# Optimization experiments

Hardware: AMD Instinct MI355X
Metric: run time of the kernel (lower is better)

## Reference

```python
import jax, jax.numpy as jnp
import numpy as np

H = 16          # num_attention_heads
D = 1024        # input_size == hidden_size
HD = D // H     # attention_head_size = 64
EPS = 1e-12


def setup_inputs() -> dict:
    key = jax.random.key(0)
    ks = jax.random.split(key, 12)
    B, S = 4, 2048
    sc = 1.0 / np.sqrt(D)
    return {
        "x": jax.random.normal(ks[0], (B, S, D), jnp.float32),
        "y": jax.random.normal(ks[1], (B, S, D), jnp.float32),
        "Wq": jax.random.normal(ks[2], (D, D), jnp.float32) * sc,
        "bq": jnp.zeros((D,), jnp.float32),
        "Wk": jax.random.normal(ks[3], (D, D), jnp.float32) * sc,
        "bk": jnp.zeros((D,), jnp.float32),
        "Wv": jax.random.normal(ks[4], (D, D), jnp.float32) * sc,
        "bv": jnp.zeros((D,), jnp.float32),
        "Wd": jax.random.normal(ks[5], (D, D), jnp.float32) * sc,
        "bd": jnp.zeros((D,), jnp.float32),
        "gamma": jnp.ones((D,), jnp.float32),
        "beta": jnp.zeros((D,), jnp.float32),
        "debug": 0,
    }


def _split_heads(t):
    B, S, _ = t.shape
    return t.reshape(B, S, H, HD).transpose(0, 2, 1, 3)  # [B,H,S,hd]


def reference(x, y, Wq, bq, Wk, bk, Wv, bv, Wd, bd, gamma, beta, debug):
    # torch Linear: t @ W.T + b
    q = _split_heads(x @ Wq.T + bq)   # query from x
    k = _split_heads(y @ Wk.T + bk)   # key from y
    v = _split_heads(x @ Wv.T + bv)   # value from x (as in source)
    scores = jnp.einsum("bhqd,bhkd->bhqk", q, k) / np.sqrt(HD)
    probs = jax.nn.softmax(scores, axis=-1)  # dropout: eval mode (identity)
    ctx = jnp.einsum("bhqk,bhkd->bhqd", probs, v)
    B, _, S, _ = ctx.shape
    ctx = ctx.transpose(0, 2, 1, 3).reshape(B, S, D)
    h = ctx @ Wd.T + bd               # out_dropout: eval mode (identity)
    h = h + x
    u = h.mean(-1, keepdims=True)
    s = jnp.square(h - u).mean(-1, keepdims=True)
    h = (h - u) / jnp.sqrt(s + EPS)
    return gamma * h + beta
```

## Files before the change

### kernel.cpp

```cpp
#include <hip/hip_runtime.h>
#include <hip/hip_bf16.h>
#include <stdint.h>


typedef unsigned short ushortT;
typedef __attribute__((ext_vector_type(8))) __bf16 bf16x8;
typedef __attribute__((ext_vector_type(4))) float f32x4;
typedef __attribute__((ext_vector_type(16))) float f32x16;
typedef __attribute__((ext_vector_type(8))) unsigned short ushort8;
typedef __attribute__((ext_vector_type(4))) unsigned short ushort4v;

__device__ __forceinline__ unsigned short f2bf(float f) {
  union { float f; unsigned u; } x; x.f = f;
  unsigned r = (x.u + 0x7FFFu + ((x.u >> 16) & 1u)) >> 16;
  return (unsigned short)r;
}

__device__ __forceinline__ unsigned cvtpk_bf16(float lo, float hi) {
  unsigned r;
  asm("v_cvt_pk_bf16_f32 %0, %1, %2" : "=v"(r) : "v"(lo), "v"(hi));
  return r;
}

__device__ __forceinline__ void load_lds16(const void* g, void* l) {
  __builtin_amdgcn_global_load_lds(
      (const __attribute__((address_space(1))) void*)g,
      (__attribute__((address_space(3))) void*)l, 16, 0, 0);
}

__device__ __forceinline__ f32x4 mfma16(bf16x8 a, bf16x8 b, f32x4 c) {
  return __builtin_amdgcn_mfma_f32_16x16x32_bf16(a, b, c, 0, 0, 0);
}
__device__ __forceinline__ f32x16 mfma32(bf16x8 a, bf16x8 b, f32x16 c) {
  return __builtin_amdgcn_mfma_f32_32x32x16_bf16(a, b, c, 0, 0, 0);
}

__global__ __launch_bounds__(256) void k_cvt_all(
    const float* __restrict__ x, const float* __restrict__ y,
    const float* __restrict__ w0, const float* __restrict__ w1,
    const float* __restrict__ w2, const float* __restrict__ w3,
    ushortT* __restrict__ ox, ushortT* __restrict__ oy,
    ushortT* __restrict__ o0, ushortT* __restrict__ o1,
    ushortT* __restrict__ o2, ushortT* __restrict__ o3) {
  int b = blockIdx.x;
  const float* in;
  ushortT* out;
  int blk;
  if (b < 4096) {
    in = x; out = ox; blk = b;
  } else if (b < 8192) {
    in = y; out = oy; blk = b - 4096;
  } else {
    int z = (b - 8192) >> 9;
    blk = (b - 8192) & 511;
    in = (z == 0) ? w0 : (z == 1) ? w1 : (z == 2) ? w2 : w3;
    out = (z == 0) ? o0 : (z == 1) ? o1 : (z == 2) ? o2 : o3;
  }
  int i = blk * 256 + threadIdx.x;
  const float4* p = (const float4*)in;
  float4 u = p[(size_t)i * 2];
  float4 v = p[(size_t)i * 2 + 1];
  ushort8 o;
  o[0] = f2bf(u.x); o[1] = f2bf(u.y); o[2] = f2bf(u.z); o[3] = f2bf(u.w);
  o[4] = f2bf(v.x); o[5] = f2bf(v.y); o[6] = f2bf(v.z); o[7] = f2bf(v.w);
  *(ushort8*)(out + (size_t)i * 8) = o;
}

__global__ __launch_bounds__(512, 4) void k_gemm(
    const ushortT* __restrict__ xbf, const ushortT* __restrict__ ybf,
    const ushortT* __restrict__ wq, const ushortT* __restrict__ wk,
    const ushortT* __restrict__ wv, const ushortT* __restrict__ wd,
    const float* __restrict__ bq, const float* __restrict__ bk,
    const float* __restrict__ bv, const float* __restrict__ bd,
    const ushortT* __restrict__ ctx, const float* __restrict__ xres,
    ushortT* __restrict__ Qo, ushortT* __restrict__ Ko,
    ushortT* __restrict__ Vt, float* __restrict__ Ho, int mode_base) {
  __shared__ ushortT lA[2][128 * 64];
  __shared__ ushortT lB[2][128 * 64];
  const int t = threadIdx.x;
  const int lane = t & 63;
  const int w = t >> 6;
  const int wm = w >> 1, wn = w & 1;
  const int mode = mode_base + blockIdx.z;
  const int flat = blockIdx.x + (blockIdx.y << 3);
  const int xcd = flat & 7, j = flat >> 3;
  const int m0 = (xcd * 8 + (j >> 3)) * 128;
  const int n0 = (j & 7) * 128;

  const ushortT* A = (mode == 1) ? ybf : (mode == 3 ? ctx : xbf);
  const ushortT* W = (mode == 0) ? wq : (mode == 1 ? wk : (mode == 2 ? wv : wd));
  const float* bias = (mode == 0) ? bq : (mode == 1 ? bk : (mode == 2 ? bv : bd));

  f32x4 z = {0.f, 0.f, 0.f, 0.f};
  f32x4 acc[2][4];
#pragma unroll
  for (int i = 0; i < 2; ++i)
#pragma unroll
    for (int j2 = 0; j2 < 4; ++j2) acc[i][j2] = z;

  const int so = t * 16;
  const int srow = so >> 7;
  const int skb = (so & 127) ^ ((srow & 7) << 4);
  const ushortT* asrc = A + (size_t)(m0 + srow) * 1024 + (skb >> 1);
  const ushortT* wsrc = W + (size_t)(n0 + srow) * 1024 + (skb >> 1);

#define GSTAGE(buf, k0)                                                     \
  do {                                                                      \
    _Pragma("unroll")                                                       \
    for (int c = 0; c < 2; ++c) {                                           \
      load_lds16(asrc + (k0) + (size_t)c * 64 * 1024,                       \
                 (char*)&lA[buf][0] + c * 8192 + t * 16);                   \
      load_lds16(wsrc + (k0) + (size_t)c * 64 * 1024,                       \
                 (char*)&lB[buf][0] + c * 8192 + t * 16);                   \
    }                                                                       \
  } while (0)

  GSTAGE(0, 0);
  __syncthreads();
  int cur = 0;
  for (int k0 = 0; k0 < 1024; k0 += 64) {
    if (k0 + 64 < 1024) GSTAGE(cur ^ 1, k0 + 64);
#pragma unroll
    for (int kk = 0; kk < 2; ++kk) {
      bf16x8 af[2], bfr[4];
#pragma unroll
      for (int i = 0; i < 2; ++i) {
        int arow = wm * 32 + i * 16 + (lane & 15);
        int ak = ((kk * 32 + (lane >> 4) * 8) * 2) ^ ((arow & 7) << 4);
        af[i] = *(const bf16x8*)((const char*)&lA[cur][0] + arow * 128 + ak);
      }
#pragma unroll
      for (int i = 0; i < 4; ++i) {
        int brow = wn * 64 + i * 16 + (lane & 15);
        int bk2 = ((kk * 32 + (lane >> 4) * 8) * 2) ^ ((brow & 7) << 4);
        bfr[i] = *(const bf16x8*)((const char*)&lB[cur][0] + brow * 128 + bk2);
      }
      __builtin_amdgcn_s_setprio(1);
#pragma unroll
      for (int i = 0; i < 2; ++i)
#pragma unroll
        for (int j2 = 0; j2 < 4; ++j2)
          acc[i][j2] = mfma16(af[i], bfr[j2], acc[i][j2]);
      __builtin_amdgcn_s_setprio(0);
    }
    __syncthreads();
    cur ^= 1;
  }
#undef GSTAGE

  const int cm = wm * 32 + (lane >> 4) * 4;
  const int cn = wn * 64 + (lane & 15);
  if (mode == 3) {
#pragma unroll
    for (int mi = 0; mi < 2; ++mi)
#pragma unroll
      for (int ni = 0; ni < 4; ++ni) {
        int n = n0 + cn + ni * 16;
        float bn = bias[n];
#pragma unroll
        for (int r = 0; r < 4; ++r) {
          int m = m0 + cm + mi * 16 + r;
          Ho[(size_t)m * 1024 + n] =
              acc[mi][ni][r] + bn + xres[(size_t)m * 1024 + n];
        }
      }
  } else if (mode == 2) {
#pragma unroll
    for (int mi = 0; mi < 2; ++mi)
#pragma unroll
      for (int ni = 0; ni < 4; ++ni) {
        int n = n0 + cn + ni * 16;
        int hh = n >> 6, hd = n & 63;
        float bn = bias[n];
        int m_ = m0 + cm + mi * 16;
        int b = m_ >> 11, s = m_ & 2047;
        ushort4v pk;
#pragma unroll
        for (int r = 0; r < 4; ++r) pk[r] = f2bf(acc[mi][ni][r] + bn);
        *(ushort4v*)&Vt[(((size_t)(b * 16 + hh) * 64 + hd) << 11) + s] = pk;
      }
  } else {
    ushortT* O = (mode == 0) ? Qo : Ko;
    const float qs = (mode == 0) ? 0.18033688011112042f : 1.0f;
#pragma unroll
    for (int mi = 0; mi < 2; ++mi)
#pragma unroll
      for (int ni = 0; ni < 4; ++ni) {
        int n = n0 + cn + ni * 16;
        int hh = n >> 6, hd = n & 63;
        float bn = bias[n];
#pragma unroll
        for (int r = 0; r < 4; ++r) {
          int m = m0 + cm + mi * 16 + r;
          int b = m >> 11, s = m & 2047;
          O[(((size_t)(b * 16 + hh) * 2048 + s) << 6) + hd] =
              f2bf((acc[mi][ni][r] + bn) * qs);
        }
      }
  }
}

__global__ __launch_bounds__(256, 4) void k_attn(const ushortT* __restrict__ Q,
                                                 const ushortT* __restrict__ K,
                                                 const ushortT* __restrict__ Vt,
                                                 ushortT* __restrict__ ctx) {
  __shared__ ushortT lK[2][4096];
  __shared__ ushortT lV[2][4096];
  const int t = threadIdx.x, lane = t & 63, w = t >> 6;
  const int hi = lane >> 5, l31 = lane & 31;
  const int i0 = blockIdx.x;
  const int xcd = i0 & 7, j0 = i0 >> 3;
  const int bh = xcd * 8 + (j0 >> 4);
  const int qt = j0 & 15;
  const int q0 = qt * 128 + w * 32;

  const ushortT* Qb = Q + ((size_t)bh * 2048 + q0) * 64;
  const ushortT* Kb = K + (size_t)bh * 2048 * 64;
  const ushortT* Vb = Vt + (size_t)bh * 64 * 2048;

  bf16x8 qf[4];
#pragma unroll
  for (int dc = 0; dc < 4; ++dc)
    qf[dc] = *(const bf16x8*)(Qb + l31 * 64 + dc * 16 + hi * 8);

  union { unsigned short us[8]; bf16x8 v; } ones_u;
#pragma unroll
  for (int i = 0; i < 8; ++i) ones_u.us[i] = 0x3F80;

  f32x16 accO0, accO1, accL;
#pragma unroll
  for (int i = 0; i < 16; ++i) { accO0[i] = 0.f; accO1[i] = 0.f; accL[i] = 0.f; }

  const int srow = t >> 3;
  const int scolb = ((t & 7) * 16) ^ ((srow & 7) << 4);
  const ushortT* ksrc = Kb + srow * 64 + (scolb >> 1);
  const ushortT* vsrc = Vb + (size_t)srow * 2048 + (scolb >> 1);
  const int swz = (lane & 7) << 4;
  const int hs = (hi * 16) ^ swz;
  const int krowb = l31 * 128;

#define STAGE(buf, kk)                                                        \
  do {                                                                        \
    load_lds16(ksrc + (size_t)(kk) * 64, (char*)&lK[buf][0] + w * 1024);      \
    load_lds16(ksrc + 2048 + (size_t)(kk) * 64,                               \
               (char*)&lK[buf][0] + 4096 + w * 1024);                         \
    load_lds16(vsrc + (kk), (char*)&lV[buf][0] + w * 1024);                   \
    load_lds16(vsrc + 65536 + (kk), (char*)&lV[buf][0] + 4096 + w * 1024);    \
  } while (0)

  STAGE(0, 0);
  __syncthreads();
  int cur = 0;
  for (int k0 = 0; k0 < 2048; k0 += 64) {
    if (k0 + 64 < 2048) STAGE(cur ^ 1, k0 + 64);
    const char* lKc = (const char*)&lK[cur][0];
    const char* lVc = (const char*)&lV[cur][0];
#pragma unroll
    for (int kb = 0; kb < 2; ++kb) {
      f32x16 sc;
#pragma unroll
      for (int i = 0; i < 16; ++i) sc[i] = 0.f;
      __builtin_amdgcn_s_setprio(1);
#pragma unroll
      for (int dc = 0; dc < 4; ++dc) {
        bf16x8 kf = *(const bf16x8*)(lKc + kb * 4096 + krowb + ((dc * 32) ^ hs));
        sc = mfma32(kf, qf[dc], sc);
      }
      __builtin_amdgcn_s_setprio(0);
      float p[16];
#pragma unroll
      for (int r = 0; r < 16; ++r) p[r] = __builtin_amdgcn_exp2f(sc[r]);
      union { unsigned u[4]; bf16x8 v; } pa0, pa1;
#pragma unroll
      for (int i = 0; i < 4; ++i) {
        int base = (i >> 1) * 8 + (i & 1) * 2;
        unsigned a = cvtpk_bf16(p[base], p[base + 1]);
        unsigned b = cvtpk_bf16(p[base + 4], p[base + 5]);
        asm("v_permlane32_swap_b32 %0, %1" : "+v"(a), "+v"(b));
        if (i >> 1) { pa1.u[i & 1] = a; pa1.u[2 + (i & 1)] = b; }
        else        { pa0.u[i & 1] = a; pa0.u[2 + (i & 1)] = b; }
      }
      __builtin_amdgcn_s_setprio(1);
#pragma unroll
      for (int nb = 0; nb < 2; ++nb) {
        const char* vrow = lVc + (nb * 32 + l31) * 128;
        bf16x8 vf0 = *(const bf16x8*)(vrow + ((kb * 64) ^ hs));
        bf16x8 vf1 = *(const bf16x8*)(vrow + ((kb * 64 + 32) ^ hs));
        f32x16& ao = nb ? accO1 : accO0;
        ao = mfma32(pa0.v, vf0, ao);
        ao = mfma32(pa1.v, vf1, ao);
      }
      accL = mfma32(pa0.v, ones_u.v, accL);
      accL = mfma32(pa1.v, ones_u.v, accL);
      __builtin_amdgcn_s_setprio(0);
    }
    __syncthreads();
    cur ^= 1;
  }
#undef STAGE

  int b = bh >> 4, hh = bh & 15;
  ushortT* cb = ctx + ((size_t)(b * 2048 + q0)) * 1024 + hh * 64;
#pragma unroll
  for (int r = 0; r < 16; ++r) {
    int qm = (r & 3) + 8 * (r >> 2) + 4 * hi;
    float lr = 1.0f / accL[r];
    size_t rb = (size_t)qm * 1024;
    cb[rb + l31] = f2bf(accO0[r] * lr);
    cb[rb + 32 + l31] = f2bf(accO1[r] * lr);
  }
}

__global__ __launch_bounds__(256) void k_ln(const float* __restrict__ Hi,
                                            const float* __restrict__ gamma,
                                            const float* __restrict__ beta,
                                            float* __restrict__ out) {
  const int row = blockIdx.x, t = threadIdx.x, lane = t & 63, w = t >> 6;
  const float4* hp = (const float4*)(Hi + (size_t)row * 1024);
  float4 v = hp[t];
  float s1 = v.x + v.y + v.z + v.w;
  float s2 = v.x * v.x + v.y * v.y + v.z * v.z + v.w * v.w;
#pragma unroll
  for (int off = 1; off < 64; off <<= 1) {
    s1 += __shfl_xor(s1, off);
    s2 += __shfl_xor(s2, off);
  }
  __shared__ float red[8];
  if (lane == 0) { red[w] = s1; red[4 + w] = s2; }
  __syncthreads();
  s1 = red[0] + red[1] + red[2] + red[3];
  s2 = red[4] + red[5] + red[6] + red[7];
  float u = s1 * (1.f / 1024.f);
  float var = s2 * (1.f / 1024.f) - u * u;
  float rstd = rsqrtf(var + 1e-12f);
  float4 g = ((const float4*)gamma)[t];
  float4 bb = ((const float4*)beta)[t];
  float4 oo;
  oo.x = (v.x - u) * rstd * g.x + bb.x;
  oo.y = (v.y - u) * rstd * g.y + bb.y;
  oo.z = (v.z - u) * rstd * g.z + bb.z;
  oo.w = (v.w - u) * rstd * g.w + bb.w;
  ((float4*)(out + (size_t)row * 1024))[t] = oo;
}

extern "C" void kernel_launch(void* const* d_in, const int* in_sizes, int n_in,
                              void* d_out, int out_size, void* d_ws,
                              size_t ws_size, hipStream_t stream) {
  const float* x = (const float*)d_in[0];
  const float* y = (const float*)d_in[1];
  const float* Wq = (const float*)d_in[2];
  const float* bq = (const float*)d_in[3];
  const float* Wk = (const float*)d_in[4];
  const float* bk = (const float*)d_in[5];
  const float* Wv = (const float*)d_in[6];
  const float* bv = (const float*)d_in[7];
  const float* Wd = (const float*)d_in[8];
  const float* bd = (const float*)d_in[9];
  const float* gamma = (const float*)d_in[10];
  const float* beta = (const float*)d_in[11];

  char* ws = (char*)d_ws;
  ushortT* xbf = (ushortT*)(ws + 0);
  ushortT* ybf = (ushortT*)(ws + 16777216);
  ushortT* wqb = (ushortT*)(ws + 33554432);
  ushortT* wkb = (ushortT*)(ws + 35651584);
  ushortT* wvb = (ushortT*)(ws + 37748736);
  ushortT* wdb = (ushortT*)(ws + 39845888);
  ushortT* Qb = (ushortT*)(ws + 41943040);
  ushortT* Kb = (ushortT*)(ws + 58720256);
  ushortT* Vtb = (ushortT*)(ws + 75497472);
  ushortT* ctx = (ushortT*)(ws + 92274688);
  float* Hbuf = (float*)(ws + 0);

  k_cvt_all<<<10240, 256, 0, stream>>>(x, y, Wq, Wk, Wv, Wd, xbf, ybf, wqb,
                                       wkb, wvb, wdb);

  k_gemm<<<dim3(8, 64, 3), 512, 0, stream>>>(xbf, ybf, wqb, wkb, wvb, wdb, bq,
                                             bk, bv, bd, ctx, x, Qb, Kb, Vtb,
                                             Hbuf, 0);
  k_attn<<<1024, 256, 0, stream>>>(Qb, Kb, Vtb, ctx);
  k_gemm<<<dim3(8, 64, 1), 512, 0, stream>>>(xbf, ybf, wqb, wkb, wvb, wdb, bq,
                                             bk, bv, bd, ctx, x, Qb, Kb, Vtb,
                                             Hbuf, 3);
  k_ln<<<8192, 256, 0, stream>>>(Hbuf, gamma, beta, (float*)d_out);
}
```

Measured before the change: 195.2 us.

## Fuse fp32-to-bf16 activation conversion into GEMM A-tile loading

Removes the separate conversion pass over x and y. The projection GEMM now loads fp32 activations into registers, converts them to bf16 with packed cvt and writes them to LDS after the MFMA loop, while weights still use direct global-to-LDS loads. This saves writing and re-reading bf16 copies of x and y. In exchange, each projection GEMM reads twice the A bytes, since x is read by both the Q and V GEMMs, and it adds register staging and VALU work inside the main loop.

```diff
diff --git a/kernel.cpp b/kernel.cpp
--- a/kernel.cpp
+++ b/kernel.cpp
@@ -35,28 +35,18 @@
   return __builtin_amdgcn_mfma_f32_32x32x16_bf16(a, b, c, 0, 0, 0);
 }
 
-__global__ __launch_bounds__(256) void k_cvt_all(
-    const float* __restrict__ x, const float* __restrict__ y,
-    const float* __restrict__ w0, const float* __restrict__ w1,
-    const float* __restrict__ w2, const float* __restrict__ w3,
-    ushortT* __restrict__ ox, ushortT* __restrict__ oy,
-    ushortT* __restrict__ o0, ushortT* __restrict__ o1,
-    ushortT* __restrict__ o2, ushortT* __restrict__ o3) {
-  int b = blockIdx.x;
-  const float* in;
-  ushortT* out;
-  int blk;
-  if (b < 4096) {
-    in = x; out = ox; blk = b;
-  } else if (b < 8192) {
-    in = y; out = oy; blk = b - 4096;
-  } else {
-    int z = (b - 8192) >> 9;
-    blk = (b - 8192) & 511;
-    in = (z == 0) ? w0 : (z == 1) ? w1 : (z == 2) ? w2 : w3;
-    out = (z == 0) ? o0 : (z == 1) ? o1 : (z == 2) ? o2 : o3;
-  }
-  int i = blk * 256 + threadIdx.x;
+__global__ __launch_bounds__(256) void k_cvtw(const float* __restrict__ w0,
+                                              const float* __restrict__ w1,
+                                              const float* __restrict__ w2,
+                                              const float* __restrict__ w3,
+                                              ushortT* __restrict__ o0,
+                                              ushortT* __restrict__ o1,
+                                              ushortT* __restrict__ o2,
+                                              ushortT* __restrict__ o3) {
+  int z = blockIdx.z;
+  const float* in = (z == 0) ? w0 : (z == 1) ? w1 : (z == 2) ? w2 : w3;
+  ushortT* out = (z == 0) ? o0 : (z == 1) ? o1 : (z == 2) ? o2 : o3;
+  int i = blockIdx.x * 256 + threadIdx.x;
   const float4* p = (const float4*)in;
   float4 u = p[(size_t)i * 2];
   float4 v = p[(size_t)i * 2 + 1];
@@ -67,7 +57,7 @@
 }
 
 __global__ __launch_bounds__(512, 4) void k_gemm(
-    const ushortT* __restrict__ xbf, const ushortT* __restrict__ ybf,
+    const float* __restrict__ xf, const float* __restrict__ yf,
     const ushortT* __restrict__ wq, const ushortT* __restrict__ wk,
     const ushortT* __restrict__ wv, const ushortT* __restrict__ wd,
     const float* __restrict__ bq, const float* __restrict__ bk,
@@ -87,7 +77,8 @@
   const int m0 = (xcd * 8 + (j >> 3)) * 128;
   const int n0 = (j & 7) * 128;
 
-  const ushortT* A = (mode == 1) ? ybf : (mode == 3 ? ctx : xbf);
+  const bool af32 = (mode != 3);
+  const float* Afp = (mode == 1) ? yf : xf;
   const ushortT* W = (mode == 0) ? wq : (mode == 1 ? wk : (mode == 2 ? wv : wd));
   const float* bias = (mode == 0) ? bq : (mode == 1 ? bk : (mode == 2 ? bv : bd));
 
@@ -101,25 +92,68 @@
   const int so = t * 16;
   const int srow = so >> 7;
   const int skb = (so & 127) ^ ((srow & 7) << 4);
-  const ushortT* asrc = A + (size_t)(m0 + srow) * 1024 + (skb >> 1);
-  const ushortT* wsrc = W + (size_t)(n0 + srow) * 1024 + (skb >> 1);
-
-#define GSTAGE(buf, k0)                                                     \
-  do {                                                                      \
-    _Pragma("unroll")                                                       \
-    for (int c = 0; c < 2; ++c) {                                           \
-      load_lds16(asrc + (k0) + (size_t)c * 64 * 1024,                       \
-                 (char*)&lA[buf][0] + c * 8192 + t * 16);                   \
-      load_lds16(wsrc + (k0) + (size_t)c * 64 * 1024,                       \
-                 (char*)&lB[buf][0] + c * 8192 + t * 16);                   \
-    }                                                                       \
+  const int se = skb >> 1;
+  const float* Afsrc = Afp + (size_t)(m0 + srow) * 1024 + se;
+  const ushortT* Absrc = ctx + (size_t)(m0 + srow) * 1024 + se;
+  const ushortT* wsrc = W + (size_t)(n0 + srow) * 1024 + se;
+
+  float4 ar[2][2];
+  ushort8 ab[2];
+
+#define AISSUE(k0)                                                          \
+  do {                                                                     \
+    _Pragma("unroll")                                                      \
+    for (int c = 0; c < 2; ++c) {                                          \
+      if (af32) {                                                          \
+        const float4* pa = (const float4*)(Afsrc + (k0) + c * 65536);      \
+        ar[c][0] = pa[0];                                                  \
+        ar[c][1] = pa[1];                                                  \
+      } else {                                                             \
+        ab[c] = *(const ushort8*)(Absrc + (k0) + c * 65536);               \
+      }                                                                    \
+    }                                                                      \
   } while (0)
 
-  GSTAGE(0, 0);
+#define AWRITE(buf)                                                        \
+  do {                                                                     \
+    _Pragma("unroll")                                                      \
+    for (int c = 0; c < 2; ++c) {                                          \
+      ushort8 o;                                                           \
+      if (af32) {                                                          \
+        unsigned w0 = cvtpk_bf16(ar[c][0].x, ar[c][0].y);                  \
+        unsigned w1 = cvtpk_bf16(ar[c][0].z, ar[c][0].w);                  \
+        unsigned w2 = cvtpk_bf16(ar[c][1].x, ar[c][1].y);                  \
+        unsigned w3 = cvtpk_bf16(ar[c][1].z, ar[c][1].w);                  \
+        o[0] = (unsigned short)w0; o[1] = (unsigned short)(w0 >> 16);      \
+        o[2] = (unsigned short)w1; o[3] = (unsigned short)(w1 >> 16);      \
+        o[4] = (unsigned short)w2; o[5] = (unsigned short)(w2 >> 16);      \
+        o[6] = (unsigned short)w3; o[7] = (unsigned short)(w3 >> 16);      \
+      } else {                                                             \
+        o = ab[c];                                                         \
+      }                                                                    \
+      *(ushort8*)((char*)&lA[buf][0] + c * 8192 + t * 16) = o;             \
+    }                                                                      \
+  } while (0)
+
+#define BSTAGE(buf, k0)                                                    \
+  do {                                                                     \
+    _Pragma("unroll")                                                      \
+    for (int c = 0; c < 2; ++c)                                            \
+      load_lds16(wsrc + (k0) + (size_t)c * 64 * 1024,                      \
+                 (char*)&lB[buf][0] + c * 8192 + t * 16);                  \
+  } while (0)
+
+  AISSUE(0);
+  BSTAGE(0, 0);
+  AWRITE(0);
   __syncthreads();
   int cur = 0;
   for (int k0 = 0; k0 < 1024; k0 += 64) {
-    if (k0 + 64 < 1024) GSTAGE(cur ^ 1, k0 + 64);
+    const bool pf = (k0 + 64 < 1024);
+    if (pf) {
+      AISSUE(k0 + 64);
+      BSTAGE(cur ^ 1, k0 + 64);
+    }
 #pragma unroll
     for (int kk = 0; kk < 2; ++kk) {
       bf16x8 af[2], bfr[4];
@@ -143,10 +177,13 @@
           acc[i][j2] = mfma16(af[i], bfr[j2], acc[i][j2]);
       __builtin_amdgcn_s_setprio(0);
     }
+    if (pf) AWRITE(cur ^ 1);
     __syncthreads();
     cur ^= 1;
   }
-#undef GSTAGE
+#undef AISSUE
+#undef AWRITE
+#undef BSTAGE
 
   const int cm = wm * 32 + (lane >> 4) * 4;
   const int cn = wn * 64 + (lane & 15);
@@ -360,8 +397,6 @@
   const float* beta = (const float*)d_in[11];
 
   char* ws = (char*)d_ws;
-  ushortT* xbf = (ushortT*)(ws + 0);
-  ushortT* ybf = (ushortT*)(ws + 16777216);
   ushortT* wqb = (ushortT*)(ws + 33554432);
   ushortT* wkb = (ushortT*)(ws + 35651584);
   ushortT* wvb = (ushortT*)(ws + 37748736);
@@ -372,15 +407,15 @@
   ushortT* ctx = (ushortT*)(ws + 92274688);
   float* Hbuf = (float*)(ws + 0);
 
-  k_cvt_all<<<10240, 256, 0, stream>>>(x, y, Wq, Wk, Wv, Wd, xbf, ybf, wqb,
-                                       wkb, wvb, wdb);
-
-  k_gemm<<<dim3(8, 64, 3), 512, 0, stream>>>(xbf, ybf, wqb, wkb, wvb, wdb, bq,
-                                             bk, bv, bd, ctx, x, Qb, Kb, Vtb,
-                                             Hbuf, 0);
+  k_cvtw<<<dim3(512, 1, 4), 256, 0, stream>>>(Wq, Wk, Wv, Wd, wqb, wkb, wvb,
+                                              wdb);
+
+  k_gemm<<<dim3(8, 64, 3), 512, 0, stream>>>(x, y, wqb, wkb, wvb, wdb, bq, bk,
+                                             bv, bd, ctx, x, Qb, Kb, Vtb, Hbuf,
+                                             0);
   k_attn<<<1024, 256, 0, stream>>>(Qb, Kb, Vtb, ctx);
-  k_gemm<<<dim3(8, 64, 1), 512, 0, stream>>>(xbf, ybf, wqb, wkb, wvb, wdb, bq,
-                                             bk, bv, bd, ctx, x, Qb, Kb, Vtb,
-                                             Hbuf, 3);
+  k_gemm<<<dim3(8, 64, 1), 512, 0, stream>>>(x, y, wqb, wkb, wvb, wdb, bq, bk,
+                                             bv, bd, ctx, x, Qb, Kb, Vtb, Hbuf,
+                                             3);
   k_ln<<<8192, 256, 0, stream>>>(Hbuf, gamma, beta, (float*)d_out);
 }
```

Result: slower. 228.1 us (+16.9%).
